# Kernel tuning notes

Hardware: AMD Instinct MI355X
Metric: run time of the kernel (lower is better)

## Reference

```python
import jax, jax.numpy as jnp
import numpy as np

N_NODES = 50000
N_EDGES = 500000
H_DIM = 128
OUT_DIM = 16
N_RELS = 90
N_BASES = 4


def setup_inputs() -> dict:
    key = jax.random.key(0)
    ks = jax.random.split(key, 12)
    inp = {
        'node_ids': jnp.arange(N_NODES, dtype=jnp.int32),
        'src': jax.random.randint(ks[0], (N_EDGES,), 0, N_NODES, dtype=jnp.int32),
        'dst': jax.random.randint(ks[1], (N_EDGES,), 0, N_NODES, dtype=jnp.int32),
        'etype': jax.random.randint(ks[2], (N_EDGES,), 0, N_RELS, dtype=jnp.int32),
        'emb': jax.random.normal(ks[3], (N_NODES, H_DIM), jnp.float32),
        'basis1': jax.random.normal(ks[4], (N_BASES, H_DIM, H_DIM), jnp.float32) * (1.0 / np.sqrt(H_DIM)),
        'comp1': jax.random.normal(ks[5], (N_RELS, N_BASES), jnp.float32) * (1.0 / np.sqrt(N_BASES)),
        'loop_w1': jax.random.normal(ks[6], (H_DIM, H_DIM), jnp.float32) * (1.0 / np.sqrt(H_DIM)),
        'bias1': jnp.zeros((H_DIM,), jnp.float32),
        'basis2': jax.random.normal(ks[7], (N_BASES, H_DIM, OUT_DIM), jnp.float32) * (1.0 / np.sqrt(H_DIM)),
        'comp2': jax.random.normal(ks[8], (N_RELS, N_BASES), jnp.float32) * (1.0 / np.sqrt(N_BASES)),
        'loop_w2': jax.random.normal(ks[9], (H_DIM, OUT_DIM), jnp.float32) * (1.0 / np.sqrt(H_DIM)),
        'bias2': jnp.zeros((OUT_DIM,), jnp.float32),
    }
    return inp


def _rel_graph_conv(x, src, dst, etype, basis, comp, loop_w, bias, num_nodes):
    # Basis decomposition: W_r = sum_b comp[r,b] * basis[b].
    # Project node features through each basis first (N is smaller than E),
    # then combine per-edge with relation coefficients: avoids per-edge GEMM.
    xb = jnp.einsum('ni,bio->nbo', x, basis)            # [N, B, out]
    msg = jnp.einsum('eb,ebo->eo', comp[etype], xb[src])  # [E, out]
    agg = jax.ops.segment_sum(msg, dst, num_segments=num_nodes)  # [N, out]
    # apply_norm=True: divide aggregated messages by in-degree of dst.
    deg = jax.ops.segment_sum(jnp.ones((src.shape[0],), x.dtype), dst,
                              num_segments=num_nodes)
    h = agg * (1.0 / jnp.maximum(deg, 1.0))[:, None]
    # self_loop=True plus bias.
    return h + x @ loop_w + bias


def reference(node_ids, src, dst, etype, emb, basis1, comp1, loop_w1, bias1,
              basis2, comp2, loop_w2, bias2):
    n = emb.shape[0]
    x = emb[node_ids]                                   # embedding lookup
    h = jax.nn.relu(_rel_graph_conv(x, src, dst, etype, basis1, comp1,
                                    loop_w1, bias1, n))
    out = _rel_graph_conv(h, src, dst, etype, basis2, comp2, loop_w2, bias2, n)
    return out
```

## Files before the change

### kernel.cpp

```cpp
#include <hip/hip_runtime.h>
#include <hip/hip_bf16.h>

#define N_NODES 50000
#define N_EDGES 500000
#define H_DIM 128
#define OUT_DIM 16
#define KDIM 640

typedef short short8 __attribute__((ext_vector_type(8)));
typedef float f32x4 __attribute__((ext_vector_type(4)));
typedef float f32x2 __attribute__((ext_vector_type(2)));

__device__ inline unsigned short f2b(float f) {
  unsigned u = __float_as_uint(f);
  u += 0x7fffu + ((u >> 16) & 1u);
  return (unsigned short)(u >> 16);
}

#define CONV_BLOCKS 6250
#define PREP_BLOCKS 360
#define INIT_BLOCKS 196
__global__ void prologue_kernel(const int* __restrict__ node_ids, const float* __restrict__ emb,
                                unsigned short* __restrict__ Abuf,
                                const float* __restrict__ basis1, const float* __restrict__ loop_w1,
                                const float* __restrict__ basis2, const float* __restrict__ loop_w2,
                                unsigned short* __restrict__ B1t, unsigned short* __restrict__ B2t,
                                int* __restrict__ cntA, int* __restrict__ cntB,
                                int* __restrict__ counter) {
  int b = blockIdx.x;
  if (b < CONV_BLOCKS) {
    int tid = b * 256 + threadIdx.x;
    if (tid >= N_NODES * (H_DIM / 4)) return;
    int n = tid >> 5;
    int q = tid & 31;
    int id = node_ids[n];
    const float4 v = *reinterpret_cast<const float4*>(emb + (size_t)id * H_DIM + q * 4);
    uint2 p;
    p.x = (unsigned)f2b(v.x) | ((unsigned)f2b(v.y) << 16);
    p.y = (unsigned)f2b(v.z) | ((unsigned)f2b(v.w) << 16);
    *reinterpret_cast<uint2*>(Abuf + (size_t)n * KDIM + 512 + q * 4) = p;
  } else if (b < CONV_BLOCKS + PREP_BLOCKS) {
    int tid = (b - CONV_BLOCKS) * 256 + threadIdx.x;
    if (tid < 128 * KDIM) {
      int c = tid / KDIM, k = tid % KDIM;
      float v = (k < 512) ? basis1[k * 128 + c] : loop_w1[(k - 512) * 128 + c];
      B1t[c * KDIM + k] = f2b(v);
    } else if (tid < 144 * KDIM) {
      int t2 = tid - 128 * KDIM;
      int c = t2 / KDIM, k = t2 % KDIM;
      float v = (k < 512) ? basis2[k * 16 + c] : loop_w2[(k - 512) * 16 + c];
      B2t[c * KDIM + k] = f2b(v);
    }
  } else {
    int i = (b - CONV_BLOCKS - PREP_BLOCKS) * 256 + threadIdx.x;
    if (i < N_NODES) {
      cntA[i] = 0;
      cntB[i] = 0;
    }
    if (i == 0) *counter = 0;
  }
}

__global__ void count_kernel(const int* __restrict__ dst, int* __restrict__ cnt) {
  for (int e = blockIdx.x * blockDim.x + threadIdx.x; e < N_EDGES; e += gridDim.x * blockDim.x)
    atomicAdd(&cnt[dst[e]], 1);
}

__global__ void alloc_kernel(const int* __restrict__ cnt, int* __restrict__ start,
                             int* __restrict__ counter) {
  int i = blockIdx.x * blockDim.x + threadIdx.x;
  int lane = threadIdx.x & 63;
  int c = (i < N_NODES) ? cnt[i] : 0;
  int incl = c;
#pragma unroll
  for (int off = 1; off < 64; off <<= 1) {
    int v = __shfl_up(incl, off, 64);
    if (lane >= off) incl += v;
  }
  int waveTotal = __shfl(incl, 63, 64);
  int base = 0;
  if (lane == 63) base = atomicAdd(counter, waveTotal);
  base = __shfl(base, 63, 64);
  if (i < N_NODES) start[i] = base + incl - c;
}

__global__ void fill_kernel(const int* __restrict__ src, const int* __restrict__ dst,
                            const int* __restrict__ et, const int* __restrict__ csr_start,
                            int* __restrict__ cnt, int2* __restrict__ csr_se) {
  for (int e = blockIdx.x * blockDim.x + threadIdx.x; e < N_EDGES; e += gridDim.x * blockDim.x) {
    int d = dst[e];
    int idx = csr_start[d] + atomicAdd(&cnt[d], 1);
    csr_se[idx] = make_int2(src[e], et[e]);
  }
}

__global__ __launch_bounds__(256) void agg_kernel(const int* __restrict__ csr_start,
                                                  const int* __restrict__ csr_cnt,
                                                  const int2* __restrict__ csr_se,
                                                  const float* __restrict__ comp,
                                                  unsigned short* __restrict__ Abuf) {
  int node = blockIdx.x * 4 + (threadIdx.x >> 6);
  if (node >= N_NODES) return;
  int lane = threadIdx.x & 63;
  int lo = __builtin_amdgcn_readfirstlane(csr_start[node]);
  int deg = __builtin_amdgcn_readfirstlane(csr_cnt[node]);
  int hi = lo + deg;

  f32x2 a0 = {0.f, 0.f}, a1 = {0.f, 0.f}, a2 = {0.f, 0.f}, a3 = {0.f, 0.f};
  const unsigned short* featb = Abuf + 512;
  const int laneoff = lane * 2;

#define EDGE_BODY(S, T)                                                              \
  {                                                                                  \
    unsigned u = *reinterpret_cast<const unsigned*>(featb + (size_t)(S)*KDIM + laneoff); \
    float4 c = *reinterpret_cast<const float4*>(comp + (T)*4);                       \
    f32x2 x;                                                                         \
    x.x = __uint_as_float(u << 16);                                                  \
    x.y = __uint_as_float(u & 0xffff0000u);                                          \
    a0 = __builtin_elementwise_fma((f32x2){c.x, c.x}, x, a0);                        \
    a1 = __builtin_elementwise_fma((f32x2){c.y, c.y}, x, a1);                        \
    a2 = __builtin_elementwise_fma((f32x2){c.z, c.z}, x, a2);                        \
    a3 = __builtin_elementwise_fma((f32x2){c.w, c.w}, x, a3);                        \
  }

  int e = lo;
  for (; e + 4 <= hi; e += 4) {
    int2 p0 = csr_se[e], p1 = csr_se[e + 1], p2 = csr_se[e + 2], p3 = csr_se[e + 3];
    int s0 = __builtin_amdgcn_readfirstlane(p0.x), t0 = __builtin_amdgcn_readfirstlane(p0.y);
    int s1 = __builtin_amdgcn_readfirstlane(p1.x), t1 = __builtin_amdgcn_readfirstlane(p1.y);
    int s2 = __builtin_amdgcn_readfirstlane(p2.x), t2 = __builtin_amdgcn_readfirstlane(p2.y);
    int s3 = __builtin_amdgcn_readfirstlane(p3.x), t3 = __builtin_amdgcn_readfirstlane(p3.y);
    EDGE_BODY(s0, t0)
    EDGE_BODY(s1, t1)
    EDGE_BODY(s2, t2)
    EDGE_BODY(s3, t3)
  }
  for (; e < hi; ++e) {
    int2 p = csr_se[e];
    int s0 = __builtin_amdgcn_readfirstlane(p.x), t0 = __builtin_amdgcn_readfirstlane(p.y);
    EDGE_BODY(s0, t0)
  }
#undef EDGE_BODY

  float inv = 1.0f / (float)(deg > 0 ? deg : 1);
  unsigned short* out = Abuf + (size_t)node * KDIM;
  unsigned p0w = (unsigned)f2b(a0.x * inv) | ((unsigned)f2b(a0.y * inv) << 16);
  unsigned p1w = (unsigned)f2b(a1.x * inv) | ((unsigned)f2b(a1.y * inv) << 16);
  unsigned p2w = (unsigned)f2b(a2.x * inv) | ((unsigned)f2b(a2.y * inv) << 16);
  unsigned p3w = (unsigned)f2b(a3.x * inv) | ((unsigned)f2b(a3.y * inv) << 16);
  *reinterpret_cast<unsigned*>(out + 0 * 128 + laneoff) = p0w;
  *reinterpret_cast<unsigned*>(out + 1 * 128 + laneoff) = p1w;
  *reinterpret_cast<unsigned*>(out + 2 * 128 + laneoff) = p2w;
  *reinterpret_cast<unsigned*>(out + 3 * 128 + laneoff) = p3w;
}

template <int NC, bool RELU, bool OUT_BF16>
__global__ __launch_bounds__(256) void gemm_kernel(const unsigned short* __restrict__ A,
                                                   const unsigned short* __restrict__ Bt,
                                                   const float* __restrict__ bias,
                                                   void* __restrict__ outp, int out_stride, int M) {
  __shared__ unsigned short As[64][64];
  __shared__ unsigned short Bs[NC][64];
  int wave = threadIdx.x >> 6;
  int lane = threadIdx.x & 63;
  int row0 = blockIdx.x * 64;
  f32x4 acc[NC / 16];
#pragma unroll
  for (int i = 0; i < NC / 16; ++i) acc[i] = (f32x4){0.f, 0.f, 0.f, 0.f};

  int ar = wave * 16 + (lane & 15);
  int kh = lane >> 4;

  for (int k0 = 0; k0 < KDIM; k0 += 64) {
#pragma unroll
    for (int p = 0; p < 2; ++p) {
      int cid = threadIdx.x + p * 256;
      int r = cid >> 3, c8 = cid & 7;
      int gr = row0 + r;
      short8 v = {};
      if (gr < M) v = *reinterpret_cast<const short8*>(A + (size_t)gr * KDIM + k0 + c8 * 8);
      *reinterpret_cast<short8*>(&As[r][(c8 ^ (r & 7)) * 8]) = v;
    }
    for (int cid = threadIdx.x; cid < NC * 8; cid += 256) {
      int r = cid >> 3, c8 = cid & 7;
      short8 v = *reinterpret_cast<const short8*>(Bt + (size_t)r * KDIM + k0 + c8 * 8);
      *reinterpret_cast<short8*>(&Bs[r][(c8 ^ (r & 7)) * 8]) = v;
    }
    __syncthreads();
    short8 a0 = *reinterpret_cast<const short8*>(&As[ar][((kh) ^ (ar & 7)) * 8]);
    short8 a1 = *reinterpret_cast<const short8*>(&As[ar][((4 + kh) ^ (ar & 7)) * 8]);
#pragma unroll
    for (int ct = 0; ct < NC / 16; ++ct) {
      int bc = ct * 16 + (lane & 15);
      short8 b0 = *reinterpret_cast<const short8*>(&Bs[bc][((kh) ^ (bc & 7)) * 8]);
      short8 b1 = *reinterpret_cast<const short8*>(&Bs[bc][((4 + kh) ^ (bc & 7)) * 8]);
      acc[ct] = __builtin_amdgcn_mfma_f32_16x16x32_bf16(a0, b0, acc[ct], 0, 0, 0);
      acc[ct] = __builtin_amdgcn_mfma_f32_16x16x32_bf16(a1, b1, acc[ct], 0, 0, 0);
    }
    __syncthreads();
  }
  int col_l = lane & 15;
  int rb = row0 + wave * 16 + (lane >> 4) * 4;
#pragma unroll
  for (int ct = 0; ct < NC / 16; ++ct) {
    int col = ct * 16 + col_l;
    float bv = bias[col];
#pragma unroll
    for (int r = 0; r < 4; ++r) {
      int gr = rb + r;
      if (gr < M) {
        float v = acc[ct][r] + bv;
        if (RELU) v = fmaxf(v, 0.0f);
        if (OUT_BF16)
          reinterpret_cast<unsigned short*>(outp)[(size_t)gr * out_stride + col] = f2b(v);
        else
          reinterpret_cast<float*>(outp)[(size_t)gr * out_stride + col] = v;
      }
    }
  }
}

extern "C" void kernel_launch(void* const* d_in, const int* in_sizes, int n_in,
                              void* d_out, int out_size, void* d_ws, size_t ws_size,
                              hipStream_t stream) {
  const int* node_ids = (const int*)d_in[0];
  const int* src = (const int*)d_in[1];
  const int* dst = (const int*)d_in[2];
  const int* etype = (const int*)d_in[3];
  const float* emb = (const float*)d_in[4];
  const float* basis1 = (const float*)d_in[5];
  const float* comp1 = (const float*)d_in[6];
  const float* loop_w1 = (const float*)d_in[7];
  const float* bias1 = (const float*)d_in[8];
  const float* basis2 = (const float*)d_in[9];
  const float* comp2 = (const float*)d_in[10];
  const float* loop_w2 = (const float*)d_in[11];
  const float* bias2 = (const float*)d_in[12];
  (void)in_sizes; (void)n_in; (void)out_size; (void)ws_size;

  char* ws = (char*)d_ws;
  size_t off = 0;
  auto alloc = [&](size_t bytes) -> void* {
    void* p = ws + off;
    off += (bytes + 255) & ~(size_t)255;
    return p;
  };
  int* csr_start = (int*)alloc(N_NODES * sizeof(int));
  int* cntA = (int*)alloc(N_NODES * sizeof(int));
  int* cntB = (int*)alloc(N_NODES * sizeof(int));
  int* counter = (int*)alloc(sizeof(int));
  int2* csr_se = (int2*)alloc((size_t)N_EDGES * sizeof(int2));
  unsigned short* Abuf = (unsigned short*)alloc((size_t)N_NODES * KDIM * sizeof(unsigned short));
  unsigned short* B1t = (unsigned short*)alloc(128 * KDIM * sizeof(unsigned short));
  unsigned short* B2t = (unsigned short*)alloc(16 * KDIM * sizeof(unsigned short));

  prologue_kernel<<<CONV_BLOCKS + PREP_BLOCKS + INIT_BLOCKS, 256, 0, stream>>>(
      node_ids, emb, Abuf, basis1, loop_w1, basis2, loop_w2, B1t, B2t, cntA, cntB, counter);
  count_kernel<<<1024, 256, 0, stream>>>(dst, cntA);
  alloc_kernel<<<(N_NODES + 255) / 256, 256, 0, stream>>>(cntA, csr_start, counter);
  fill_kernel<<<1024, 256, 0, stream>>>(src, dst, etype, csr_start, cntB, csr_se);

  agg_kernel<<<(N_NODES + 3) / 4, 256, 0, stream>>>(csr_start, cntA, csr_se, comp1, Abuf);
  gemm_kernel<128, true, true><<<(N_NODES + 63) / 64, 256, 0, stream>>>(
      Abuf, B1t, bias1, Abuf + 512, KDIM, N_NODES);

  agg_kernel<<<(N_NODES + 3) / 4, 256, 0, stream>>>(csr_start, cntA, csr_se, comp2, Abuf);
  gemm_kernel<16, false, false><<<(N_NODES + 63) / 64, 256, 0, stream>>>(
      Abuf, B2t, bias2, d_out, OUT_DIM, N_NODES);
}
```

Before: 175.7 us.

## Project layer-2 features through bases before aggregation to shrink edge gather width

For the second layer, the per-node hidden features are now projected through the four bases and the self-loop weight first. This uses one GEMM producing 80 bf16 columns, written back into the activation buffer. A new aggregation kernel then gathers only 64 bf16 values per edge, combines them with relation coefficients via lane shuffles, and adds the self-loop term and bias. This replaces the old layer-2 aggregation over 128-wide features plus the K=640 GEMM, cutting per-edge gather traffic and GEMM K. The cost is an extra bf16 rounding of projected features before the edge sum.

```diff
diff --git a/kernel.cpp b/kernel.cpp
--- a/kernel.cpp
+++ b/kernel.cpp
@@ -15,6 +15,9 @@
   unsigned u = __float_as_uint(f);
   u += 0x7fffu + ((u >> 16) & 1u);
   return (unsigned short)(u >> 16);
+}
+__device__ inline float b2f(unsigned short u) {
+  return __uint_as_float(((unsigned)u) << 16);
 }
 
 #define CONV_BLOCKS 6250
@@ -24,7 +27,7 @@
                                 unsigned short* __restrict__ Abuf,
                                 const float* __restrict__ basis1, const float* __restrict__ loop_w1,
                                 const float* __restrict__ basis2, const float* __restrict__ loop_w2,
-                                unsigned short* __restrict__ B1t, unsigned short* __restrict__ B2t,
+                                unsigned short* __restrict__ B1t, unsigned short* __restrict__ B2pt,
                                 int* __restrict__ cntA, int* __restrict__ cntB,
                                 int* __restrict__ counter) {
   int b = blockIdx.x;
@@ -45,11 +48,12 @@
       int c = tid / KDIM, k = tid % KDIM;
       float v = (k < 512) ? basis1[k * 128 + c] : loop_w1[(k - 512) * 128 + c];
       B1t[c * KDIM + k] = f2b(v);
-    } else if (tid < 144 * KDIM) {
+    } else if (tid < 128 * KDIM + 80 * 128) {
       int t2 = tid - 128 * KDIM;
-      int c = t2 / KDIM, k = t2 % KDIM;
-      float v = (k < 512) ? basis2[k * 16 + c] : loop_w2[(k - 512) * 16 + c];
-      B2t[c * KDIM + k] = f2b(v);
+      int c = t2 / 128, k = t2 % 128;
+      float v = (c < 64) ? basis2[(c >> 4) * 128 * 16 + k * 16 + (c & 15)]
+                         : loop_w2[k * 16 + (c - 64)];
+      B2pt[c * 128 + k] = f2b(v);
     }
   } else {
     int i = (b - CONV_BLOCKS - PREP_BLOCKS) * 256 + threadIdx.x;
@@ -154,11 +158,70 @@
   *reinterpret_cast<unsigned*>(out + 3 * 128 + laneoff) = p3w;
 }
 
-template <int NC, bool RELU, bool OUT_BF16>
+__global__ __launch_bounds__(256) void agg2_kernel(const int* __restrict__ csr_start,
+                                                   const int* __restrict__ csr_cnt,
+                                                   const int2* __restrict__ csr_se,
+                                                   const float* __restrict__ comp,
+                                                   const unsigned short* __restrict__ Abuf,
+                                                   const float* __restrict__ bias2,
+                                                   float* __restrict__ dout) {
+  int node = blockIdx.x * 4 + (threadIdx.x >> 6);
+  if (node >= N_NODES) return;
+  int lane = threadIdx.x & 63;
+  int bsel = lane >> 4;
+  int o = lane & 15;
+  int lo = __builtin_amdgcn_readfirstlane(csr_start[node]);
+  int deg = __builtin_amdgcn_readfirstlane(csr_cnt[node]);
+  int hi = lo + deg;
+
+  float acc = 0.f;
+
+#define EDGE2_BODY(S, T)                                                   \
+  {                                                                        \
+    unsigned short u = Abuf[(size_t)(S)*KDIM + lane];                      \
+    float4 c = *reinterpret_cast<const float4*>(comp + (T)*4);             \
+    float cb = (bsel < 2) ? ((bsel == 0) ? c.x : c.y)                      \
+                          : ((bsel == 2) ? c.z : c.w);                     \
+    acc = fmaf(cb, b2f(u), acc);                                           \
+  }
+
+  int e = lo;
+  for (; e + 4 <= hi; e += 4) {
+    int2 p0 = csr_se[e], p1 = csr_se[e + 1], p2 = csr_se[e + 2], p3 = csr_se[e + 3];
+    int s0 = __builtin_amdgcn_readfirstlane(p0.x), t0 = __builtin_amdgcn_readfirstlane(p0.y);
+    int s1 = __builtin_amdgcn_readfirstlane(p1.x), t1 = __builtin_amdgcn_readfirstlane(p1.y);
+    int s2 = __builtin_amdgcn_readfirstlane(p2.x), t2 = __builtin_amdgcn_readfirstlane(p2.y);
+    int s3 = __builtin_amdgcn_readfirstlane(p3.x), t3 = __builtin_amdgcn_readfirstlane(p3.y);
+    EDGE2_BODY(s0, t0)
+    EDGE2_BODY(s1, t1)
+    EDGE2_BODY(s2, t2)
+    EDGE2_BODY(s3, t3)
+  }
+  for (; e < hi; ++e) {
+    int2 p = csr_se[e];
+    int s0 = __builtin_amdgcn_readfirstlane(p.x), t0 = __builtin_amdgcn_readfirstlane(p.y);
+    EDGE2_BODY(s0, t0)
+  }
+#undef EDGE2_BODY
+
+  acc += __shfl_xor(acc, 16, 64);
+  acc += __shfl_xor(acc, 32, 64);
+
+  if (lane < 16) {
+    float inv = 1.0f / (float)(deg > 0 ? deg : 1);
+    float sl = b2f(Abuf[(size_t)node * KDIM + 64 + o]);
+    dout[(size_t)node * OUT_DIM + o] = acc * inv + sl + bias2[o];
+  }
+}
+
+template <int NC, int KT, bool RELU, bool HAS_BIAS>
 __global__ __launch_bounds__(256) void gemm_kernel(const unsigned short* __restrict__ A,
+                                                   int a_stride,
                                                    const unsigned short* __restrict__ Bt,
+                                                   int bt_stride,
                                                    const float* __restrict__ bias,
-                                                   void* __restrict__ outp, int out_stride, int M) {
+                                                   unsigned short* __restrict__ outp,
+                                                   int out_stride, int M) {
   __shared__ unsigned short As[64][64];
   __shared__ unsigned short Bs[NC][64];
   int wave = threadIdx.x >> 6;
@@ -171,19 +234,19 @@
   int ar = wave * 16 + (lane & 15);
   int kh = lane >> 4;
 
-  for (int k0 = 0; k0 < KDIM; k0 += 64) {
+  for (int k0 = 0; k0 < KT; k0 += 64) {
 #pragma unroll
     for (int p = 0; p < 2; ++p) {
       int cid = threadIdx.x + p * 256;
       int r = cid >> 3, c8 = cid & 7;
       int gr = row0 + r;
       short8 v = {};
-      if (gr < M) v = *reinterpret_cast<const short8*>(A + (size_t)gr * KDIM + k0 + c8 * 8);
+      if (gr < M) v = *reinterpret_cast<const short8*>(A + (size_t)gr * a_stride + k0 + c8 * 8);
       *reinterpret_cast<short8*>(&As[r][(c8 ^ (r & 7)) * 8]) = v;
     }
     for (int cid = threadIdx.x; cid < NC * 8; cid += 256) {
       int r = cid >> 3, c8 = cid & 7;
-      short8 v = *reinterpret_cast<const short8*>(Bt + (size_t)r * KDIM + k0 + c8 * 8);
+      short8 v = *reinterpret_cast<const short8*>(Bt + (size_t)r * bt_stride + k0 + c8 * 8);
       *reinterpret_cast<short8*>(&Bs[r][(c8 ^ (r & 7)) * 8]) = v;
     }
     __syncthreads();
@@ -204,17 +267,14 @@
 #pragma unroll
   for (int ct = 0; ct < NC / 16; ++ct) {
     int col = ct * 16 + col_l;
-    float bv = bias[col];
+    float bv = HAS_BIAS ? bias[col] : 0.f;
 #pragma unroll
     for (int r = 0; r < 4; ++r) {
       int gr = rb + r;
       if (gr < M) {
         float v = acc[ct][r] + bv;
         if (RELU) v = fmaxf(v, 0.0f);
-        if (OUT_BF16)
-          reinterpret_cast<unsigned short*>(outp)[(size_t)gr * out_stride + col] = f2b(v);
-        else
-          reinterpret_cast<float*>(outp)[(size_t)gr * out_stride + col] = v;
+        outp[(size_t)gr * out_stride + col] = f2b(v);
       }
     }
   }
@@ -252,19 +312,20 @@
   int2* csr_se = (int2*)alloc((size_t)N_EDGES * sizeof(int2));
   unsigned short* Abuf = (unsigned short*)alloc((size_t)N_NODES * KDIM * sizeof(unsigned short));
   unsigned short* B1t = (unsigned short*)alloc(128 * KDIM * sizeof(unsigned short));
-  unsigned short* B2t = (unsigned short*)alloc(16 * KDIM * sizeof(unsigned short));
+  unsigned short* B2pt = (unsigned short*)alloc(80 * 128 * sizeof(unsigned short));
 
   prologue_kernel<<<CONV_BLOCKS + PREP_BLOCKS + INIT_BLOCKS, 256, 0, stream>>>(
-      node_ids, emb, Abuf, basis1, loop_w1, basis2, loop_w2, B1t, B2t, cntA, cntB, counter);
+      node_ids, emb, Abuf, basis1, loop_w1, basis2, loop_w2, B1t, B2pt, cntA, cntB, counter);
   count_kernel<<<1024, 256, 0, stream>>>(dst, cntA);
   alloc_kernel<<<(N_NODES + 255) / 256, 256, 0, stream>>>(cntA, csr_start, counter);
   fill_kernel<<<1024, 256, 0, stream>>>(src, dst, etype, csr_start, cntB, csr_se);
 
   agg_kernel<<<(N_NODES + 3) / 4, 256, 0, stream>>>(csr_start, cntA, csr_se, comp1, Abuf);
-  gemm_kernel<128, true, true><<<(N_NODES + 63) / 64, 256, 0, stream>>>(
-      Abuf, B1t, bias1, Abuf + 512, KDIM, N_NODES);
-
-  agg_kernel<<<(N_NODES + 3) / 4, 256, 0, stream>>>(csr_start, cntA, csr_se, comp2, Abuf);
-  gemm_kernel<16, false, false><<<(N_NODES + 63) / 64, 256, 0, stream>>>(
-      Abuf, B2t, bias2, d_out, OUT_DIM, N_NODES);
-}
+  gemm_kernel<128, KDIM, true, true><<<(N_NODES + 63) / 64, 256, 0, stream>>>(
+      Abuf, KDIM, B1t, KDIM, bias1, Abuf + 512, KDIM, N_NODES);
+
+  gemm_kernel<80, 128, false, false><<<(N_NODES + 63) / 64, 256, 0, stream>>>(
+      Abuf + 512, KDIM, B2pt, 128, nullptr, Abuf, KDIM, N_NODES);
+  agg2_kernel<<<(N_NODES + 3) / 4, 256, 0, stream>>>(csr_start, cntA, csr_se, comp2, Abuf,
+                                                     bias2, (float*)d_out);
+}
```

Result: faster. 166.9 us (-5.0%).
